# Kernel optimization log

Measured on AMD Instinct MI355X. Metric: run time of the kernel, lower is better.

The kernel has to match this reference:

```python
import jax, jax.numpy as jnp
import numpy as np

B, C_IN, C_OUT, H, W = 2, 64, 32, 80, 80


def conv1x1(x, w, b):
    # x: [B, Cin, H, W], w: [Cout, Cin], b: [Cout]
    return jnp.einsum('bchw,oc->bohw', x, w) + b[None, :, None, None]


def setup_inputs() -> dict:
    key = jax.random.key(0)
    ks = jax.random.split(key, 5)
    scale = 0.02  # keep dot products moderate since exp() is unscaled (no max-subtract)
    return {
        'input_x': jax.random.normal(ks[0], (B, C_IN, H, W), dtype=jnp.float32),
        'w_g': jax.random.normal(ks[1], (C_OUT, C_IN), dtype=jnp.float32) * scale,
        'b_g': jnp.zeros((C_OUT,), dtype=jnp.float32),
        'w_phi': jax.random.normal(ks[2], (C_OUT, C_IN), dtype=jnp.float32) * scale,
        'b_phi': jnp.zeros((C_OUT,), dtype=jnp.float32),
        'w_theta': jax.random.normal(ks[3], (C_OUT, C_IN), dtype=jnp.float32) * scale,
        'b_theta': jnp.zeros((C_OUT,), dtype=jnp.float32),
        'w_y': jax.random.normal(ks[4], (C_IN, C_OUT), dtype=jnp.float32) * scale,
        'b_y': jnp.zeros((C_IN,), dtype=jnp.float32),
    }


def reference(input_x, w_g, b_g, w_phi, b_phi, w_theta, b_theta, w_y, b_y):
    batch = input_x.shape[0]
    g = conv1x1(input_x, w_g, b_g)          # [B, Cout, H, W]
    phi = conv1x1(input_x, w_phi, b_phi)    # [B, Cout, H, W]
    theta = conv1x1(input_x, w_theta, b_theta)
    # Faithful to torch: raw reshape (row-major reinterpretation), NOT a transpose
    g_x = g.reshape(batch, -1, C_OUT)        # [B, HW, Cout]
    theta_x = theta.reshape(batch, -1, C_OUT)
    phi_x = phi.reshape(batch, -1, C_OUT)
    f = jnp.einsum('bnc,bmc->bnm', theta_x, phi_x)  # [B, HW, HW]
    # nltype=0: unscaled exp / row-sum normalization (no max subtraction, faithful)
    f = jnp.exp(f)
    f_softmax = f / jnp.sum(f, axis=-1, keepdims=True)
    y = jnp.einsum('bnm,bmc->bnc', f_softmax, g_x)  # [B, HW, Cout]
    y = y.reshape(batch, C_OUT, H, W)
    z = conv1x1(y, w_y, b_y)                 # [B, Cin, H, W]
    return z
```

## Files before the change

kernel.cpp:

```cpp
#include <hip/hip_runtime.h>
#include <hip/hip_bf16.h>

#define BATCH 2
#define CIN   64
#define COUT  32
#define HW    6400
#define PB    (COUT*HW)
#define XB    (CIN*HW)
#define KSPLIT 5
#define LOG2E 1.4426950408889634f

typedef __attribute__((ext_vector_type(8))) short  bf16x8;
typedef __attribute__((ext_vector_type(4))) float  f32x4;

typedef unsigned short ushort;
typedef unsigned int   uint;

__device__ inline uint pk2(float a, float b) {
  __hip_bfloat162 h = __float22bfloat162_rn(make_float2(a, b));
  union { __hip_bfloat162 h2; uint u; } cv; cv.h2 = h;
  return cv.u;
}
__device__ inline float up_lo(uint u) { return __uint_as_float(u << 16); }

#define MFMA16(a, bop, c) __builtin_amdgcn_mfma_f32_16x16x32_bf16((a), (bop), (c), 0, 0, 0)

__global__ __launch_bounds__(128) void conv3_kernel(
    const float* __restrict__ x,
    const float* __restrict__ w0, const float* __restrict__ bb0,
    const float* __restrict__ w1, const float* __restrict__ bb1,
    const float* __restrict__ w2, const float* __restrict__ bb2,
    ushort* __restrict__ T_hi, ushort* __restrict__ T_lo,
    ushort* __restrict__ P_hi, ushort* __restrict__ Gt_hi) {
  const int which = blockIdx.y >> 1;
  const int oh    = blockIdx.y & 1;
  const float* w  = (which == 0) ? w0 : (which == 1) ? w1 : w2;
  const float* bv = (which == 0) ? bb0 : (which == 1) ? bb1 : bb2;
  const int b = blockIdx.z;
  const int s = blockIdx.x * 128 + threadIdx.x;

  __shared__ float wsm[16 * CIN];
  for (int i = threadIdx.x; i < 16 * CIN; i += 128)
    wsm[i] = w[oh * 16 * CIN + i];
  __syncthreads();

  float xr[CIN];
#pragma unroll
  for (int c = 0; c < CIN; ++c) xr[c] = x[b * XB + c * HW + s];

  for (int oi = 0; oi < 16; ++oi) {
    const int o = oh * 16 + oi;
    const float4* wr = (const float4*)&wsm[oi * CIN];
    float acc = 0.f;
#pragma unroll
    for (int q = 0; q < CIN / 4; ++q) {
      float4 wv = wr[q];
      acc += wv.x * xr[4*q] + wv.y * xr[4*q+1] + wv.z * xr[4*q+2] + wv.w * xr[4*q+3];
    }
    acc += bv[o];
    if (which == 0) acc *= LOG2E;
    uint hb = pk2(acc, 0.f) & 0xFFFFu;
    if (which == 2) {
      const int m  = o * 200 + (s >> 5);
      const int np = (m & ~31) + 16*((m>>3)&1) + 8*((m>>2)&1)
                   + 4*((m>>4)&1) + (m & 3);
      Gt_hi[b * PB + (s & 31) * HW + np] = (ushort)hb;
    } else {
      const int f = b * PB + o * HW + s;
      if (which == 0) {
        T_hi[f] = (ushort)hb;
        float hf = up_lo(hb);
        T_lo[f] = (ushort)(pk2(acc - hf, 0.f) & 0xFFFFu);
      } else {
        P_hi[f] = (ushort)hb;
      }
    }
  }
}

__global__ __launch_bounds__(256, 3) void attn_kernel(
    const ushort* __restrict__ T_hi, const ushort* __restrict__ T_lo,
    const ushort* __restrict__ P_hi, const ushort* __restrict__ Gt_hi,
    float* __restrict__ Yp,
    float* __restrict__ Dp) {
  const int b     = blockIdx.z;
  const int ks    = blockIdx.y;
  const int q_blk = blockIdx.x;
  const int tid   = threadIdx.x;
  const int w     = tid >> 6;
  const int lane  = tid & 63;
  const int l15   = lane & 15;
  const int g     = lane >> 4;

  __shared__ float yl[4 * 32 * 33 + 4 * 32];

  const int niter = 10;
  const int kbase = ks * 1280 + w * 32;

  bf16x8 t_hi[4], t_lo[4];
#pragma unroll
  for (int s2 = 0; s2 < 4; ++s2) {
    const int qrow = q_blk * 64 + s2 * 16 + l15;
    t_hi[s2] = *(const bf16x8*)&T_hi[b * PB + qrow * 32 + g * 8];
    t_lo[s2] = *(const bf16x8*)&T_lo[b * PB + qrow * 32 + g * 8];
  }

  const ushort* pg = P_hi + b * PB + (kbase + l15) * 32 + g * 8;
  const ushort* gg = Gt_hi + b * PB + l15 * HW + kbase + g * 8;

  f32x4 acc0[4] = {{0,0,0,0},{0,0,0,0},{0,0,0,0},{0,0,0,0}};
  f32x4 acc1[4] = {{0,0,0,0},{0,0,0,0},{0,0,0,0},{0,0,0,0}};
  float denom[4] = {0.f, 0.f, 0.f, 0.f};

  bf16x8 pa = *(const bf16x8*)pg;
  bf16x8 pb = *(const bf16x8*)(pg + 512);
  bf16x8 g0 = *(const bf16x8*)gg;
  bf16x8 g1 = *(const bf16x8*)(gg + 16 * HW);

  for (int i = 0; i < niter; ++i) {
    bf16x8 pan, pbn, g0n, g1n;
    if (i + 1 < niter) {
      const ushort* pgn = pg + (i + 1) * 4096;
      const ushort* ggn = gg + (i + 1) * 128;
      pan = *(const bf16x8*)pgn;
      pbn = *(const bf16x8*)(pgn + 512);
      g0n = *(const bf16x8*)ggn;
      g1n = *(const bf16x8*)(ggn + 16 * HW);
    }

#pragma unroll
    for (int s2 = 0; s2 < 4; ++s2) {
      f32x4 sa = {0.f,0.f,0.f,0.f};
      f32x4 sb = {0.f,0.f,0.f,0.f};
      __builtin_amdgcn_s_setprio(1);
      sa = MFMA16(pa, t_hi[s2], sa);
      sa = MFMA16(pa, t_lo[s2], sa);
      sb = MFMA16(pb, t_hi[s2], sb);
      sb = MFMA16(pb, t_lo[s2], sb);
      __builtin_amdgcn_s_setprio(0);

      const float ea0 = __builtin_amdgcn_exp2f(sa[0]);
      const float ea1 = __builtin_amdgcn_exp2f(sa[1]);
      const float ea2 = __builtin_amdgcn_exp2f(sa[2]);
      const float ea3 = __builtin_amdgcn_exp2f(sa[3]);
      const float eb0 = __builtin_amdgcn_exp2f(sb[0]);
      const float eb1 = __builtin_amdgcn_exp2f(sb[1]);
      const float eb2 = __builtin_amdgcn_exp2f(sb[2]);
      const float eb3 = __builtin_amdgcn_exp2f(sb[3]);
      denom[s2] += ((ea0 + ea1) + (ea2 + ea3)) + ((eb0 + eb1) + (eb2 + eb3));

      union { uint u[4]; bf16x8 v; } ph;
      ph.u[0] = pk2(ea0, ea1); ph.u[1] = pk2(ea2, ea3);
      ph.u[2] = pk2(eb0, eb1); ph.u[3] = pk2(eb2, eb3);

      __builtin_amdgcn_s_setprio(1);
      acc0[s2] = MFMA16(ph.v, g0, acc0[s2]);
      acc1[s2] = MFMA16(ph.v, g1, acc1[s2]);
      __builtin_amdgcn_s_setprio(0);
    }

    if (i + 1 < niter) { pa = pan; pb = pbn; g0 = g0n; g1 = g1n; }
  }

  float* dl = yl + 4 * 32 * 33;
  const int c  = tid & 31;
  const int q0 = tid >> 5;

#pragma unroll
  for (int p = 0; p < 2; ++p) {
    __syncthreads();
#pragma unroll
    for (int sl = 0; sl < 2; ++sl) {
      const int s2 = p * 2 + sl;
      float dn = denom[s2];
      dn += __shfl_xor(dn, 16);
      dn += __shfl_xor(dn, 32);
#pragma unroll
      for (int r = 0; r < 4; ++r) {
        yl[(w * 32 + sl * 16 + 4 * g + r) * 33 + l15]      = acc0[s2][r];
        yl[(w * 32 + sl * 16 + 4 * g + r) * 33 + 16 + l15] = acc1[s2][r];
      }
      if (g == 0) dl[w * 32 + sl * 16 + l15] = dn;
    }
    __syncthreads();

#pragma unroll
    for (int rr = 0; rr < 4; ++rr) {
      const int row = rr * 8 + q0;
      float y = 0.f, d = 0.f;
#pragma unroll
      for (int k2 = 0; k2 < 4; ++k2) {
        y += yl[(k2 * 32 + row) * 33 + c];
        d += dl[k2 * 32 + row];
      }
      const int qrow = q_blk * 64 + p * 32 + row;
      Yp[((size_t)(ks * BATCH + b)) * PB + qrow * 32 + c] = y;
      if (c == 0) Dp[((size_t)(ks * BATCH + b)) * HW + qrow] = d;
    }
  }
}

__global__ __launch_bounds__(128) void conv_out_kernel(
    const float* __restrict__ Yp, const float* __restrict__ Dp,
    const float* __restrict__ wy, const float* __restrict__ by,
    float* __restrict__ z) {
  const int b  = blockIdx.z;
  const int ih = blockIdx.y;
  const int s  = blockIdx.x * 128 + threadIdx.x;

  __shared__ float wsm[32 * COUT];
  for (int i = threadIdx.x; i < 32 * COUT; i += 128)
    wsm[i] = wy[ih * 32 * COUT + i];
  __syncthreads();

  float yr[COUT];
#pragma unroll
  for (int o = 0; o < COUT; ++o) {
    const int f = o * HW + s;
    const int n = f >> 5;
    float y = 0.f, d = 0.f;
#pragma unroll
    for (int ksi = 0; ksi < KSPLIT; ++ksi) {
      y += Yp[((size_t)(ksi * BATCH + b)) * PB + f];
      d += Dp[((size_t)(ksi * BATCH + b)) * HW + n];
    }
    yr[o] = y / d;
  }

  for (int ii = 0; ii < 32; ++ii) {
    const int i = ih * 32 + ii;
    const float4* wr = (const float4*)&wsm[ii * COUT];
    float acc = 0.f;
#pragma unroll
    for (int q = 0; q < COUT / 4; ++q) {
      float4 wv = wr[q];
      acc += wv.x * yr[4*q] + wv.y * yr[4*q+1] + wv.z * yr[4*q+2] + wv.w * yr[4*q+3];
    }
    z[(size_t)b * XB + i * HW + s] = acc + by[i];
  }
}

extern "C" void kernel_launch(void* const* d_in, const int* in_sizes, int n_in,
                              void* d_out, int out_size, void* d_ws, size_t ws_size,
                              hipStream_t stream) {
  const float* x       = (const float*)d_in[0];
  const float* w_g     = (const float*)d_in[1];
  const float* b_g     = (const float*)d_in[2];
  const float* w_phi   = (const float*)d_in[3];
  const float* b_phi   = (const float*)d_in[4];
  const float* w_theta = (const float*)d_in[5];
  const float* b_theta = (const float*)d_in[6];
  const float* w_y     = (const float*)d_in[7];
  const float* b_y     = (const float*)d_in[8];
  float* z = (float*)d_out;

  char* base = (char*)d_ws;
  const size_t BF = (size_t)BATCH * PB * sizeof(ushort);
  ushort* T_hi  = (ushort*)(base);
  ushort* T_lo  = (ushort*)(base + 1 * BF);
  ushort* P_hi  = (ushort*)(base + 2 * BF);
  ushort* Gt_hi = (ushort*)(base + 3 * BF);
  float*  Yp    = (float*)(base + 4 * BF);
  float*  Dp    = (float*)(base + 4 * BF +
                           (size_t)KSPLIT * BATCH * PB * sizeof(float));

  conv3_kernel<<<dim3(50, 6, BATCH), 128, 0, stream>>>(
      x, w_theta, b_theta, w_phi, b_phi, w_g, b_g,
      T_hi, T_lo, P_hi, Gt_hi);
  attn_kernel<<<dim3(100, KSPLIT, BATCH), 256, 0, stream>>>(
      T_hi, T_lo, P_hi, Gt_hi, Yp, Dp);
  conv_out_kernel<<<dim3(50, 2, BATCH), 128, 0, stream>>>(Yp, Dp, w_y, b_y, z);
}
```

Measured before the change: 57.13 us.

## Drop theta low-part bf16 correction and double attention key split

Removes the hi/lo bf16 split of theta, so the score computation uses a single bf16 MFMA per tile instead of two, and T_lo is no longer written or read. It also raises the key-dimension split from 5 to 10 so more blocks run, each covering half the keys, and drops the s_setprio hints around the MFMAs. This cuts score-MFMA work and memory traffic. The cost is lower precision in the exponent argument, which is unscaled and not max-subtracted, and twice as many partial Y and denominator buffers for the output kernel to reduce.

```diff
diff --git a/kernel.cpp b/kernel.cpp
--- a/kernel.cpp
+++ b/kernel.cpp
@@ -7,7 +7,7 @@
 #define HW    6400
 #define PB    (COUT*HW)
 #define XB    (CIN*HW)
-#define KSPLIT 5
+#define KSPLIT 10
 #define LOG2E 1.4426950408889634f
 
 typedef __attribute__((ext_vector_type(8))) short  bf16x8;
@@ -21,7 +21,6 @@
   union { __hip_bfloat162 h2; uint u; } cv; cv.h2 = h;
   return cv.u;
 }
-__device__ inline float up_lo(uint u) { return __uint_as_float(u << 16); }
 
 #define MFMA16(a, bop, c) __builtin_amdgcn_mfma_f32_16x16x32_bf16((a), (bop), (c), 0, 0, 0)
 
@@ -30,8 +29,8 @@
     const float* __restrict__ w0, const float* __restrict__ bb0,
     const float* __restrict__ w1, const float* __restrict__ bb1,
     const float* __restrict__ w2, const float* __restrict__ bb2,
-    ushort* __restrict__ T_hi, ushort* __restrict__ T_lo,
-    ushort* __restrict__ P_hi, ushort* __restrict__ Gt_hi) {
+    ushort* __restrict__ T_hi, ushort* __restrict__ P_hi,
+    ushort* __restrict__ Gt_hi) {
   const int which = blockIdx.y >> 1;
   const int oh    = blockIdx.y & 1;
   const float* w  = (which == 0) ? w0 : (which == 1) ? w1 : w2;
@@ -59,28 +58,22 @@
     }
     acc += bv[o];
     if (which == 0) acc *= LOG2E;
-    uint hb = pk2(acc, 0.f) & 0xFFFFu;
+    const ushort hb = (ushort)(pk2(acc, 0.f) & 0xFFFFu);
     if (which == 2) {
       const int m  = o * 200 + (s >> 5);
       const int np = (m & ~31) + 16*((m>>3)&1) + 8*((m>>2)&1)
                    + 4*((m>>4)&1) + (m & 3);
-      Gt_hi[b * PB + (s & 31) * HW + np] = (ushort)hb;
+      Gt_hi[b * PB + (s & 31) * HW + np] = hb;
     } else {
       const int f = b * PB + o * HW + s;
-      if (which == 0) {
-        T_hi[f] = (ushort)hb;
-        float hf = up_lo(hb);
-        T_lo[f] = (ushort)(pk2(acc - hf, 0.f) & 0xFFFFu);
-      } else {
-        P_hi[f] = (ushort)hb;
-      }
+      if (which == 0) T_hi[f] = hb; else P_hi[f] = hb;
     }
   }
 }
 
 __global__ __launch_bounds__(256, 3) void attn_kernel(
-    const ushort* __restrict__ T_hi, const ushort* __restrict__ T_lo,
-    const ushort* __restrict__ P_hi, const ushort* __restrict__ Gt_hi,
+    const ushort* __restrict__ T_hi, const ushort* __restrict__ P_hi,
+    const ushort* __restrict__ Gt_hi,
     float* __restrict__ Yp,
     float* __restrict__ Dp) {
   const int b     = blockIdx.z;
@@ -94,15 +87,14 @@
 
   __shared__ float yl[4 * 32 * 33 + 4 * 32];
 
-  const int niter = 10;
-  const int kbase = ks * 1280 + w * 32;
-
-  bf16x8 t_hi[4], t_lo[4];
+  const int niter = 640 / 128;
+  const int kbase = ks * 640 + w * 32;
+
+  bf16x8 t_hi[4];
 #pragma unroll
   for (int s2 = 0; s2 < 4; ++s2) {
     const int qrow = q_blk * 64 + s2 * 16 + l15;
     t_hi[s2] = *(const bf16x8*)&T_hi[b * PB + qrow * 32 + g * 8];
-    t_lo[s2] = *(const bf16x8*)&T_lo[b * PB + qrow * 32 + g * 8];
   }
 
   const ushort* pg = P_hi + b * PB + (kbase + l15) * 32 + g * 8;
@@ -132,12 +124,8 @@
     for (int s2 = 0; s2 < 4; ++s2) {
       f32x4 sa = {0.f,0.f,0.f,0.f};
       f32x4 sb = {0.f,0.f,0.f,0.f};
-      __builtin_amdgcn_s_setprio(1);
       sa = MFMA16(pa, t_hi[s2], sa);
-      sa = MFMA16(pa, t_lo[s2], sa);
       sb = MFMA16(pb, t_hi[s2], sb);
-      sb = MFMA16(pb, t_lo[s2], sb);
-      __builtin_amdgcn_s_setprio(0);
 
       const float ea0 = __builtin_amdgcn_exp2f(sa[0]);
       const float ea1 = __builtin_amdgcn_exp2f(sa[1]);
@@ -153,10 +141,8 @@
       ph.u[0] = pk2(ea0, ea1); ph.u[1] = pk2(ea2, ea3);
       ph.u[2] = pk2(eb0, eb1); ph.u[3] = pk2(eb2, eb3);
 
-      __builtin_amdgcn_s_setprio(1);
       acc0[s2] = MFMA16(ph.v, g0, acc0[s2]);
       acc1[s2] = MFMA16(ph.v, g1, acc1[s2]);
-      __builtin_amdgcn_s_setprio(0);
     }
 
     if (i + 1 < niter) { pa = pan; pb = pbn; g0 = g0n; g1 = g1n; }
@@ -257,17 +243,16 @@
   char* base = (char*)d_ws;
   const size_t BF = (size_t)BATCH * PB * sizeof(ushort);
   ushort* T_hi  = (ushort*)(base);
-  ushort* T_lo  = (ushort*)(base + 1 * BF);
-  ushort* P_hi  = (ushort*)(base + 2 * BF);
-  ushort* Gt_hi = (ushort*)(base + 3 * BF);
-  float*  Yp    = (float*)(base + 4 * BF);
-  float*  Dp    = (float*)(base + 4 * BF +
+  ushort* P_hi  = (ushort*)(base + 1 * BF);
+  ushort* Gt_hi = (ushort*)(base + 2 * BF);
+  float*  Yp    = (float*)(base + 3 * BF);
+  float*  Dp    = (float*)(base + 3 * BF +
                            (size_t)KSPLIT * BATCH * PB * sizeof(float));
 
   conv3_kernel<<<dim3(50, 6, BATCH), 128, 0, stream>>>(
       x, w_theta, b_theta, w_phi, b_phi, w_g, b_g,
-      T_hi, T_lo, P_hi, Gt_hi);
+      T_hi, P_hi, Gt_hi);
   attn_kernel<<<dim3(100, KSPLIT, BATCH), 256, 0, stream>>>(
-      T_hi, T_lo, P_hi, Gt_hi, Yp, Dp);
+      T_hi, P_hi, Gt_hi, Yp, Dp);
   conv_out_kernel<<<dim3(50, 2, BATCH), 128, 0, stream>>>(Yp, Dp, w_y, b_y, z);
 }
```

New measurement: 57.93 us. Within noise of the previous version (+1.4%).
